# Optimization experiments

Measured on AMD Instinct MI355X. Metric: run time of the kernel, lower is better.

## Reference

```python
import jax, jax.numpy as jnp
import numpy as np
jax.config.update("jax_enable_x64", True)

B, N, FEAT_DIM, OUT_DIM = 16, 10000, 256, 256
CH = [3, 64, 64, 64, 128, FEAT_DIM]  # ptlk PointNet_features MLP widths (scale=1)
BN_EPS = 1e-5
L2_EPS = 1e-12


def setup_inputs() -> dict:
    key = jax.random.key(0)
    ks = jax.random.split(key, 2 * len(CH) + 4)
    inp = {"points": jax.random.normal(ks[0], (B, N, 3), dtype=jnp.float32)}
    for i in range(5):
        cin, cout = CH[i], CH[i + 1]
        inp[f"W{i}"] = jax.random.normal(ks[1 + 2 * i], (cout, cin), dtype=jnp.float32) / np.sqrt(cin).astype(np.float32)
        inp[f"g{i}"] = jnp.ones((cout,), jnp.float32)
        inp[f"b{i}"] = jnp.zeros((cout,), jnp.float32)
    inp["Wfc"] = jax.random.normal(ks[-2], (OUT_DIM, FEAT_DIM * FEAT_DIM), dtype=jnp.float32) / np.sqrt(FEAT_DIM * FEAT_DIM).astype(np.float32)
    inp["bfc"] = jnp.zeros((OUT_DIM,), jnp.float32)
    return inp


def _bn_relu(y, g, b):
    # training-mode BatchNorm1d over (batch, points) per channel; y: [B,C,N]
    mu = jnp.mean(y, axis=(0, 2), keepdims=True)
    var = jnp.var(y, axis=(0, 2), keepdims=True)
    y = (y - mu) * jax.lax.rsqrt(var + BN_EPS)
    return jax.nn.relu(y * g[None, :, None] + b[None, :, None])


def reference(points, W0, g0, b0, W1, g1, b1, W2, g2, b2, W3, g3, b3, W4, g4, b4, Wfc, bfc):
    x = jnp.transpose(points, (0, 2, 1))  # [B,3,N]
    for W, g, b in ((W0, g0, b0), (W1, g1, b1), (W2, g2, b2), (W3, g3, b3), (W4, g4, b4)):
        x = jnp.einsum('oc,bcn->bon', W, x)  # 1x1 conv1d
        x = _bn_relu(x, g, b)
    f = jnp.transpose(x, (0, 2, 1))  # [B,N,D] per-point features
    # so_cov: global mean over all B*N points (as in the original), then per-batch covariance
    mean = jnp.mean(f.reshape(-1, FEAT_DIM), axis=0)  # [D]
    fc = f - mean
    cov = jnp.einsum('bnd,bne->bde', fc, fc) / np.float32(N)  # [B,D,D]
    # matrix square-root via fp64 SVD (torch: x.double(); u s v = svd; u diag(s^0.5) v^T)
    u, s, vh = jnp.linalg.svd(cov.astype(jnp.float64), full_matrices=False)
    sqrt_cov = (u * jnp.sqrt(s)[:, None, :]) @ vh  # [B,D,D]
    v = sqrt_cov.reshape(f.shape[0], FEAT_DIM * FEAT_DIM).astype(jnp.float32)
    out = v @ Wfc.T + bfc  # [B,OUT_DIM]
    norm = jnp.maximum(jnp.linalg.norm(out, axis=-1, keepdims=True), L2_EPS)
    return out / norm
```

## Files before the change

kernel.cpp:

```cpp
#include <hip/hip_runtime.h>
#include <cmath>

constexpr int NB   = 16;
constexpr int NPTS = 10000;
constexpr int NBN  = NB * NPTS;
constexpr int NS_ITERS = 18;
constexpr int COV_CHUNKS = 20;
constexpr int CHUNK_PTS  = 500;
constexpr int COV_KK     = 16;

typedef _Float16 f16x8 __attribute__((ext_vector_type(8)));
typedef float  f32x4  __attribute__((ext_vector_type(4)));
typedef unsigned short ushort4v __attribute__((ext_vector_type(4)));
typedef unsigned short ushort8v __attribute__((ext_vector_type(8)));

__global__ __launch_bounds__(256) void conv0_ker(const float* __restrict__ pts,
                                                 const float* __restrict__ W,
                                                 float* __restrict__ y) {
    int g = blockIdx.x * 256 + threadIdx.x;
    int b = g / NPTS;
    int n = g - b * NPTS;
    float p0 = pts[3 * (size_t)g + 0];
    float p1 = pts[3 * (size_t)g + 1];
    float p2 = pts[3 * (size_t)g + 2];
    float* yp = y + ((size_t)b * 64) * NPTS + n;
    for (int o = 0; o < 64; ++o) {
        float v = W[3 * o] * p0 + W[3 * o + 1] * p1 + W[3 * o + 2] * p2;
        yp[(size_t)o * NPTS] = v;
    }
}

__device__ __forceinline__ unsigned short f2h(float f) {
    return __builtin_bit_cast(unsigned short, (_Float16)f);
}
__device__ __forceinline__ float hres(float f) {
    return f - (float)(_Float16)f;
}
__device__ __forceinline__ int swzu(int us) {
    return us ^ (((us >> 7) & 3) << 4);
}
__device__ __forceinline__ int swz8(int byteoff) {
    return byteoff ^ (((byteoff >> 8) & 3) << 5);
}

template <int CIN, int COUT, int OTILE>
__global__ __launch_bounds__(256) void conv_mfma(const float* __restrict__ xin,
                                                 const float* __restrict__ ss,
                                                 const float* __restrict__ W,
                                                 float* __restrict__ y,
                                                 float* __restrict__ stats) {
    constexpr int OT = OTILE / 16;
    constexpr int WM = 4;
    constexpr int WN = (OTILE == 128) ? 4 : 2;
    constexpr int NCW = (OTILE == 128) ? 2 : 4;
    __shared__ unsigned short Xp[2][8 * 512];
    __shared__ unsigned short Wp[2][OT * 512];

    const int tid  = threadIdx.x;
    const int lane = tid & 63;
    const int w    = tid >> 6;
    const int wr   = (OTILE == 128) ? (w & 1) : 0;
    const int wc   = (OTILE == 128) ? (w >> 1) : w;

    const int nb = blockIdx.x * 128;
    const int ob = blockIdx.y * OTILE;
    const int b  = blockIdx.z;

    f32x4 acc[WM][WN];
#pragma unroll
    for (int m = 0; m < WM; ++m)
#pragma unroll
        for (int n = 0; n < WN; ++n) acc[m][n] = (f32x4){0.f, 0.f, 0.f, 0.f};

    const int xn = tid & 127;
    const int th = tid >> 7;
    const bool nok = (nb + xn) < NPTS;

    float xv[2][8];
    {
        const float* xb0 = xin + ((size_t)(b * CIN)) * NPTS + nb + xn;
#pragma unroll
        for (int qq = 0; qq < 2; ++qq) {
            int q = th * 2 + qq;
#pragma unroll
            for (int j = 0; j < 8; ++j)
                xv[qq][j] = nok ? xb0[(size_t)(q * 8 + j) * NPTS] : 0.f;
        }
    }

#pragma unroll 1
    for (int kc = 0; kc < CIN; kc += 32) {
        __builtin_amdgcn_sched_barrier(0);
        __builtin_amdgcn_s_barrier();
        __builtin_amdgcn_sched_barrier(0);
#pragma unroll
        for (int i = 0; i < OTILE / 32; ++i) {
            int l = i * 256 + tid;
            int o = l >> 3, k4 = (l & 7) << 2;
            float4 v = *(const float4*)(W + (size_t)(ob + o) * CIN + kc + k4);
            ushort4v h4, l4;
            h4[0] = f2h(v.x); l4[0] = f2h(hres(v.x));
            h4[1] = f2h(v.y); l4[1] = f2h(hres(v.y));
            h4[2] = f2h(v.z); l4[2] = f2h(hres(v.z));
            h4[3] = f2h(v.w); l4[3] = f2h(hres(v.w));
            int us = swzu((o >> 4) * 512 + ((k4 >> 3) * 16 + (o & 15)) * 8 + (k4 & 7));
            *(ushort4v*)&Wp[0][us] = h4;
            *(ushort4v*)&Wp[1][us] = l4;
        }
#pragma unroll
        for (int qq = 0; qq < 2; ++qq) {
            int q = th * 2 + qq;
            float f[8];
#pragma unroll
            for (int j = 0; j < 8; ++j) {
                int c = kc + q * 8 + j;
                f[j] = fmaxf(fmaf(xv[qq][j], ss[c], ss[256 + c]), 0.f);
            }
            ushort8v h8, l8;
#pragma unroll
            for (int j = 0; j < 8; ++j) {
                h8[j] = f2h(f[j]);
                l8[j] = f2h(hres(f[j]));
            }
            int us = swzu((xn >> 4) * 512 + (q * 16 + (xn & 15)) * 8);
            *(ushort8v*)&Xp[0][us] = h8;
            *(ushort8v*)&Xp[1][us] = l8;
        }
        if (kc + 32 < CIN) {
            const float* xb0 = xin + ((size_t)(b * CIN + kc + 32)) * NPTS + nb + xn;
#pragma unroll
            for (int qq = 0; qq < 2; ++qq) {
                int q = th * 2 + qq;
#pragma unroll
                for (int j = 0; j < 8; ++j)
                    xv[qq][j] = nok ? xb0[(size_t)(q * 8 + j) * NPTS] : 0.f;
            }
        }
        asm volatile("s_waitcnt lgkmcnt(0)" ::: "memory");
        __builtin_amdgcn_s_barrier();
        __builtin_amdgcn_sched_barrier(0);

        f16x8 ah[WM], al[WM], bh[WN], bl[WN];
#pragma unroll
        for (int m = 0; m < WM; ++m) {
            int us = swzu((wr * WM + m) * 512 + lane * 8);
            ah[m] = *(const f16x8*)&Wp[0][us];
            al[m] = *(const f16x8*)&Wp[1][us];
        }
#pragma unroll
        for (int n = 0; n < WN; ++n) {
            int us = swzu((wc * WN + n) * 512 + lane * 8);
            bh[n] = *(const f16x8*)&Xp[0][us];
            bl[n] = *(const f16x8*)&Xp[1][us];
        }
#pragma unroll
        for (int m = 0; m < WM; ++m)
#pragma unroll
            for (int n = 0; n < WN; ++n) {
                acc[m][n] = __builtin_amdgcn_mfma_f32_16x16x32_f16(ah[m], bh[n], acc[m][n], 0, 0, 0);
                acc[m][n] = __builtin_amdgcn_mfma_f32_16x16x32_f16(ah[m], bl[n], acc[m][n], 0, 0, 0);
                acc[m][n] = __builtin_amdgcn_mfma_f32_16x16x32_f16(al[m], bh[n], acc[m][n], 0, 0, 0);
            }
    }

    const int ro = (lane >> 4) * 4;
    const int co = lane & 15;
#pragma unroll
    for (int m = 0; m < WM; ++m) {
        int o = ob + wr * (WM * 16) + m * 16 + ro;
#pragma unroll
        for (int n = 0; n < WN; ++n) {
            int col = nb + wc * (WN * 16) + n * 16 + co;
            if (col < NPTS) {
                float* yp = y + ((size_t)(b * COUT + o)) * NPTS + col;
#pragma unroll
                for (int r = 0; r < 4; ++r)
                    yp[(size_t)r * NPTS] = acc[m][n][r];
            }
        }
    }

    __syncthreads();
    float* sbuf = (float*)&Xp[0][0];
    float* qbuf = sbuf + NCW * OTILE;
#pragma unroll
    for (int m = 0; m < WM; ++m)
#pragma unroll
        for (int r = 0; r < 4; ++r) {
            float s = 0.f, q = 0.f;
#pragma unroll
            for (int n = 0; n < WN; ++n) {
                int col = nb + wc * (WN * 16) + n * 16 + co;
                float v = acc[m][n][r];
                if (col < NPTS) { s += v; q = fmaf(v, v, q); }
            }
            s += __shfl_xor(s, 1); q += __shfl_xor(q, 1);
            s += __shfl_xor(s, 2); q += __shfl_xor(q, 2);
            s += __shfl_xor(s, 4); q += __shfl_xor(q, 4);
            s += __shfl_xor(s, 8); q += __shfl_xor(q, 8);
            if (co == 0) {
                int rowl = wr * (WM * 16) + m * 16 + ro + r;
                sbuf[wc * OTILE + rowl] = s;
                qbuf[wc * OTILE + rowl] = q;
            }
        }
    __syncthreads();
    if (tid < OTILE) {
        float s = 0.f, q = 0.f;
#pragma unroll
        for (int j = 0; j < NCW; ++j) {
            s += sbuf[j * OTILE + tid];
            q += qbuf[j * OTILE + tid];
        }
        atomicAdd(&stats[ob + tid], s);
        atomicAdd(&stats[COUT + ob + tid], q);
    }
}

__global__ void chan_stats(const float* __restrict__ y, int C, float* __restrict__ stats) {
    int c = blockIdx.x, b = blockIdx.y, t = threadIdx.x;
    const float* p = y + ((size_t)(b * C + c)) * NPTS;
    float s = 0.f, q = 0.f;
    for (int n = t; n < NPTS; n += 256) {
        float v = p[n];
        s += v;
        q = fmaf(v, v, q);
    }
    for (int off = 32; off; off >>= 1) {
        s += __shfl_down(s, off);
        q += __shfl_down(q, off);
    }
    __shared__ float ls[4], lq[4];
    if ((t & 63) == 0) { ls[t >> 6] = s; lq[t >> 6] = q; }
    __syncthreads();
    if (t == 0) {
        atomicAdd(&stats[c],     ls[0] + ls[1] + ls[2] + ls[3]);
        atomicAdd(&stats[C + c], lq[0] + lq[1] + lq[2] + lq[3]);
    }
}

__global__ void bn_finalize(const float* __restrict__ stats, const float* __restrict__ g,
                            const float* __restrict__ bi, int C, float* __restrict__ ss) {
    int c = threadIdx.x;
    if (c < C) {
        float mu  = stats[c] * (1.f / NBN);
        float var = stats[C + c] * (1.f / NBN) - mu * mu;
        float r = rsqrtf(var + 1e-5f);
        float s = g[c] * r;
        ss[c] = s;
        ss[256 + c] = bi[c] - mu * s;
    }
}

template <int NPAN>
__device__ __forceinline__ void cov_issue(const float* __restrict__ y4, int b,
                                          int ti, int tj, int chb, int p4,
                                          int n0c, int kk, float4 (&cur)[NPAN][4]) {
    const int nbase = n0c + kk * 32;
#pragma unroll
    for (int p = 0; p < NPAN; ++p) {
        const int pcb = (p ? tj : ti) * 128;
#pragma unroll
        for (int i = 0; i < 4; ++i) {
            const int ch = chb + 32 * i;
            float4 v = make_float4(0.f, 0.f, 0.f, 0.f);
            if (kk * 32 + p4 < CHUNK_PTS)
                v = *(const float4*)(y4 + ((size_t)(b * 256 + pcb + ch)) * NPTS + nbase + p4);
            cur[p][i] = v;
        }
    }
}

template <int NPAN>
__global__ __launch_bounds__(256) void cov_mfma(const float* __restrict__ y4,
                                                const float* __restrict__ ss,
                                                float* __restrict__ covP,
                                                float* __restrict__ fsumb) {
    __shared__ unsigned short pan[NPAN][2][4096];

    const int chunk = blockIdx.x;
    const int tile  = (NPAN == 2) ? 2 : (int)blockIdx.y;
    const int b     = blockIdx.z;
    const int ti = (tile == 1) ? 1 : 0;
    const int tj = (tile == 0) ? 0 : 1;

    const int tid  = threadIdx.x;
    const int lane = tid & 63;
    const int w    = tid >> 6;
    const int wr   = w & 1, wc = w >> 1;
    const int n0c  = chunk * CHUNK_PTS;

    f32x4 acc[4][4];
#pragma unroll
    for (int m = 0; m < 4; ++m)
#pragma unroll
        for (int n = 0; n < 4; ++n) acc[m][n] = (f32x4){0.f, 0.f, 0.f, 0.f};

    const int g   = tid & 7;
    const int chb = tid >> 3;
    const int p4  = g * 4;
    const int q   = p4 >> 3, j0 = p4 & 7;

    float fs[4] = {0.f, 0.f, 0.f, 0.f};
    float4 cur[NPAN][4];

    cov_issue<NPAN>(y4, b, ti, tj, chb, p4, n0c, 0, cur);

#pragma unroll 1
    for (int kk = 0; kk < COV_KK; ++kk) {
        __builtin_amdgcn_sched_barrier(0);
        __builtin_amdgcn_s_barrier();
        __builtin_amdgcn_sched_barrier(0);

        const bool ok = (kk * 32 + p4 < CHUNK_PTS);
#pragma unroll
        for (int p = 0; p < NPAN; ++p) {
            const int pcb = (p ? tj : ti) * 128;
#pragma unroll
            for (int i = 0; i < 4; ++i) {
                const int ch = chb + 32 * i;
                float4 v = cur[p][i];
                if (ok) {
                    float sc = ss[pcb + ch], sh = ss[256 + pcb + ch];
                    v.x = fmaxf(fmaf(v.x, sc, sh), 0.f);
                    v.y = fmaxf(fmaf(v.y, sc, sh), 0.f);
                    v.z = fmaxf(fmaf(v.z, sc, sh), 0.f);
                    v.w = fmaxf(fmaf(v.w, sc, sh), 0.f);
                } else {
                    v = make_float4(0.f, 0.f, 0.f, 0.f);
                }
                if (NPAN == 1) fs[i] += (v.x + v.y) + (v.z + v.w);
                ushort4v h4, l4;
                h4[0] = f2h(v.x); l4[0] = f2h(hres(v.x));
                h4[1] = f2h(v.y); l4[1] = f2h(hres(v.y));
                h4[2] = f2h(v.z); l4[2] = f2h(hres(v.z));
                h4[3] = f2h(v.w); l4[3] = f2h(hres(v.w));
                const int addr = (ch >> 4) * 512 + (q * 16 + (ch & 15)) * 8 + j0;
                const int sa = swz8(addr * 2) >> 1;
                *(ushort4v*)&pan[p][0][sa] = h4;
                *(ushort4v*)&pan[p][1][sa] = l4;
            }
        }
        if (kk + 1 < COV_KK)
            cov_issue<NPAN>(y4, b, ti, tj, chb, p4, n0c, kk + 1, cur);

        asm volatile("s_waitcnt lgkmcnt(0)" ::: "memory");
        __builtin_amdgcn_s_barrier();
        __builtin_amdgcn_sched_barrier(0);

        const unsigned short* Ah = pan[0][0];
        const unsigned short* Al = pan[0][1];
        const unsigned short* Bh = pan[NPAN - 1][0];
        const unsigned short* Bl = pan[NPAN - 1][1];

        f16x8 ah[4], al[4], bh[4], bl[4];
#pragma unroll
        for (int m = 0; m < 4; ++m) {
            int t8 = (wr * 4 + m) * 512 + lane * 8;
            int sa = swz8(t8 * 2) >> 1;
            ah[m] = *(const f16x8*)&Ah[sa];
            al[m] = *(const f16x8*)&Al[sa];
        }
#pragma unroll
        for (int n = 0; n < 4; ++n) {
            int t8 = (wc * 4 + n) * 512 + lane * 8;
            int sa = swz8(t8 * 2) >> 1;
            bh[n] = *(const f16x8*)&Bh[sa];
            bl[n] = *(const f16x8*)&Bl[sa];
        }
#pragma unroll
        for (int m = 0; m < 4; ++m)
#pragma unroll
            for (int n = 0; n < 4; ++n) {
                acc[m][n] = __builtin_amdgcn_mfma_f32_16x16x32_f16(ah[m], bh[n], acc[m][n], 0, 0, 0);
                acc[m][n] = __builtin_amdgcn_mfma_f32_16x16x32_f16(ah[m], bl[n], acc[m][n], 0, 0, 0);
                acc[m][n] = __builtin_amdgcn_mfma_f32_16x16x32_f16(al[m], bh[n], acc[m][n], 0, 0, 0);
            }
    }

    if (NPAN == 1) {
#pragma unroll
        for (int i = 0; i < 4; ++i) {
            float s = fs[i];
            s += __shfl_xor(s, 1);
            s += __shfl_xor(s, 2);
            s += __shfl_xor(s, 4);
            if (g == 0)
                atomicAdd(&fsumb[b * 256 + ti * 128 + chb + 32 * i], s);
        }
    }

    float* outp = covP + (((size_t)(chunk * NB + b) * 3 + tile) << 14);
    const int rowb = wr * 64;
    const int colb = wc * 64;
#pragma unroll
    for (int m = 0; m < 4; ++m)
#pragma unroll
        for (int n = 0; n < 4; ++n)
#pragma unroll
            for (int r = 0; r < 4; ++r) {
                int row = rowb + m * 16 + (lane >> 4) * 4 + r;
                int col = colb + n * 16 + (lane & 15);
                outp[(row << 7) + col] = acc[m][n][r];
            }
}

__global__ void covfin_ker(const float* __restrict__ covP, const float* __restrict__ fsumb,
                           float* __restrict__ Y0, float* __restrict__ trace) {
    int r = blockIdx.x, b = blockIdx.y, c = threadIdx.x;
    float fbr = fsumb[b * 256 + r] * (1.f / NPTS);
    float fbc = fsumb[b * 256 + c] * (1.f / NPTS);
    float mr = 0.f, mc = 0.f;
    for (int q = 0; q < NB; ++q) {
        mr += fsumb[q * 256 + r];
        mc += fsumb[q * 256 + c];
    }
    mr *= (1.f / NBN);
    mc *= (1.f / NBN);
    int tile, rr, cc;
    if (r < 128 && c < 128)        { tile = 0; rr = r;       cc = c; }
    else if (r >= 128 && c >= 128) { tile = 1; rr = r - 128; cc = c - 128; }
    else if (r < 128)              { tile = 2; rr = r;       cc = c - 128; }
    else                           { tile = 2; rr = c;       cc = r - 128; }
    size_t base = (((size_t)b * 3 + tile) << 14) + ((size_t)rr << 7) + cc;
    float m5 = 0.f;
#pragma unroll
    for (int q = 0; q < COV_CHUNKS; ++q)
        m5 += covP[(size_t)q * (NB * 3 * 16384) + base];
    float v = m5 * (1.f / NPTS) - fbr * mc - mr * fbc + mr * mc;
    Y0[((size_t)b << 16) + ((size_t)r << 8) + c] = v;
    if (c == r) atomicAdd(&trace[b], v);
}

__global__ void ns_init(float* __restrict__ Y0, float* __restrict__ Z0,
                        const float* __restrict__ trace) {
    int i = blockIdx.x * 256 + threadIdx.x;
    int b = i >> 16, rc = i & 65535;
    float inv = 1.f / trace[b];
    Y0[i] *= inv;
    Z0[i] = ((rc >> 8) == (rc & 255)) ? 1.f : 0.f;
}

__device__ __forceinline__ void ns_body8(const float* __restrict__ Ab,
                                         const float* __restrict__ Bb,
                                         float* __restrict__ Ob,
                                         float scale, float diag, int tile, int tid,
                                         unsigned short* Ap0, unsigned short* Ap1,
                                         unsigned short* Bp0, unsigned short* Bp1) {
    const int lane = tid & 63;
    const int w    = tid >> 6;
    const int wr   = w & 3;
    const int wc   = w >> 2;
    const int tr = (tile >> 2) * 64, tc = (tile & 3) * 64;

    f32x4 acc[2];
    acc[0] = (f32x4){0.f, 0.f, 0.f, 0.f};
    acc[1] = (f32x4){0.f, 0.f, 0.f, 0.f};

    const int r2   = tid >> 3;
    const int kq8  = tid & 7;
    const int colB = tid & 63;
    const int kB   = tid >> 6;

#pragma unroll 1
    for (int kc = 0; kc < 256; kc += 64) {
        __syncthreads();
        {
            const float* ap = Ab + (size_t)(tr + r2) * 256 + kc + kq8 * 8;
            float av[8];
            *(float4*)&av[0] = *(const float4*)ap;
            *(float4*)&av[4] = *(const float4*)(ap + 4);
            ushort8v h8, l8;
#pragma unroll
            for (int j = 0; j < 8; ++j) { h8[j] = f2h(av[j]); l8[j] = f2h(hres(av[j])); }
            const int ua = ((r2 >> 4) * 2 + (kq8 >> 2)) * 512 + ((kq8 & 3) * 16 + (r2 & 15)) * 8;
            const int sa = swz8(ua * 2) >> 1;
            *(ushort8v*)&Ap0[sa] = h8;
            *(ushort8v*)&Ap1[sa] = l8;
        }
        {
            const float* bp = Bb + (size_t)(kc + kB * 8) * 256 + tc + colB;
            float bv[8];
#pragma unroll
            for (int j = 0; j < 8; ++j) bv[j] = bp[(size_t)j * 256];
            ushort8v h8, l8;
#pragma unroll
            for (int j = 0; j < 8; ++j) { h8[j] = f2h(bv[j]); l8[j] = f2h(hres(bv[j])); }
            const int ub = ((colB >> 4) * 2 + (kB >> 2)) * 512 + ((kB & 3) * 16 + (colB & 15)) * 8;
            const int sb = swz8(ub * 2) >> 1;
            *(ushort8v*)&Bp0[sb] = h8;
            *(ushort8v*)&Bp1[sb] = l8;
        }
        __syncthreads();

#pragma unroll
        for (int kk = 0; kk < 2; ++kk) {
            const int ua = swz8(((wr * 2 + kk) * 512 + lane * 8) * 2) >> 1;
            f16x8 a_h = *(const f16x8*)&Ap0[ua];
            f16x8 a_l = *(const f16x8*)&Ap1[ua];
#pragma unroll
            for (int n = 0; n < 2; ++n) {
                const int ub = swz8((((wc * 2 + n) * 2 + kk) * 512 + lane * 8) * 2) >> 1;
                f16x8 b_h = *(const f16x8*)&Bp0[ub];
                f16x8 b_l = *(const f16x8*)&Bp1[ub];
                acc[n] = __builtin_amdgcn_mfma_f32_16x16x32_f16(a_h, b_h, acc[n], 0, 0, 0);
                acc[n] = __builtin_amdgcn_mfma_f32_16x16x32_f16(a_h, b_l, acc[n], 0, 0, 0);
                acc[n] = __builtin_amdgcn_mfma_f32_16x16x32_f16(a_l, b_h, acc[n], 0, 0, 0);
            }
        }
    }

    const int ro = (lane >> 4) * 4, co = lane & 15;
#pragma unroll
    for (int n = 0; n < 2; ++n) {
        int row = tr + wr * 16 + ro;
        int col = tc + wc * 32 + n * 16 + co;
#pragma unroll
        for (int r = 0; r < 4; ++r) {
            float v = scale * acc[n][r] + (((row + r) == col) ? diag : 0.f);
            Ob[(size_t)(row + r) * 256 + col] = v;
        }
    }
}

__global__ __launch_bounds__(512) void ns_gemm(const float* __restrict__ A,
                                               const float* __restrict__ B,
                                               float* __restrict__ O,
                                               float scale, float diag) {
    __shared__ unsigned short Ap[2][4096], Bp[2][4096];
    size_t off = (size_t)blockIdx.y << 16;
    ns_body8(A + off, B + off, O + off, scale, diag, blockIdx.x, threadIdx.x,
             Ap[0], Ap[1], Bp[0], Bp[1]);
}

__global__ __launch_bounds__(512) void ns_gemm_pair(const float* __restrict__ Y,
                                                    const float* __restrict__ Mm,
                                                    const float* __restrict__ Z,
                                                    float* __restrict__ Yn,
                                                    float* __restrict__ Zn) {
    __shared__ unsigned short Ap[2][4096], Bp[2][4096];
    size_t off = (size_t)blockIdx.y << 16;
    if (blockIdx.z == 0)
        ns_body8(Y + off, Mm + off, Yn + off, 0.5f, 0.f, blockIdx.x, threadIdx.x,
                 Ap[0], Ap[1], Bp[0], Bp[1]);
    else
        ns_body8(Mm + off, Z + off, Zn + off, 0.5f, 0.f, blockIdx.x, threadIdx.x,
                 Ap[0], Ap[1], Bp[0], Bp[1]);
}

__global__ __launch_bounds__(256) void fc_ker(const float* __restrict__ Yf,
                                              const float* __restrict__ trace,
                                              const float* __restrict__ Wfc,
                                              float* __restrict__ outpre) {
    int kc = blockIdx.x;
    int ot = blockIdx.y;
    int t = threadIdx.x;
    __shared__ float Wl[64][129];
    __shared__ float Vl[16][129];
#pragma unroll
    for (int i = 0; i < 32; ++i) {
        int l = i * 256 + t;
        int o = l >> 7, k = l & 127;
        Wl[o][k] = Wfc[(size_t)(ot * 64 + o) * 65536 + kc * 128 + k];
    }
#pragma unroll
    for (int i = 0; i < 8; ++i) {
        int l = i * 256 + t;
        int bb = l >> 7, k = l & 127;
        Vl[bb][k] = sqrtf(trace[bb]) * Yf[((size_t)bb << 16) + kc * 128 + k];
    }
    __syncthreads();
    int ol = t & 63, bg = t >> 6;
    float a0 = 0.f, a1 = 0.f, a2 = 0.f, a3 = 0.f;
    for (int k = 0; k < 128; ++k) {
        float w = Wl[ol][k];
        a0 = fmaf(w, Vl[bg * 4 + 0][k], a0);
        a1 = fmaf(w, Vl[bg * 4 + 1][k], a1);
        a2 = fmaf(w, Vl[bg * 4 + 2][k], a2);
        a3 = fmaf(w, Vl[bg * 4 + 3][k], a3);
    }
    int o = ot * 64 + ol;
    atomicAdd(&outpre[(bg * 4 + 0) * 256 + o], a0);
    atomicAdd(&outpre[(bg * 4 + 1) * 256 + o], a1);
    atomicAdd(&outpre[(bg * 4 + 2) * 256 + o], a2);
    atomicAdd(&outpre[(bg * 4 + 3) * 256 + o], a3);
}

__global__ void norm_ker(const float* __restrict__ outpre, const float* __restrict__ bfc,
                         float* __restrict__ dout) {
    int b = blockIdx.x, t = threadIdx.x;
    float v = outpre[b * 256 + t] + bfc[t];
    float q = v * v;
    for (int off = 32; off; off >>= 1) q += __shfl_xor(q, off);
    __shared__ float lq[4];
    __shared__ float snorm;
    if ((t & 63) == 0) lq[t >> 6] = q;
    __syncthreads();
    if (t == 0) snorm = fmaxf(sqrtf(lq[0] + lq[1] + lq[2] + lq[3]), 1e-12f);
    __syncthreads();
    dout[b * 256 + t] = v / snorm;
}

extern "C" void kernel_launch(void* const* d_in, const int* in_sizes, int n_in,
                              void* d_out, int out_size, void* d_ws, size_t ws_size,
                              hipStream_t stream) {
    (void)in_sizes; (void)n_in; (void)out_size; (void)ws_size;
    const float* pts = (const float*)d_in[0];
    const float* Wm[5]; const float* gm[5]; const float* bm[5];
    for (int i = 0; i < 5; ++i) {
        Wm[i] = (const float*)d_in[1 + 3 * i];
        gm[i] = (const float*)d_in[2 + 3 * i];
        bm[i] = (const float*)d_in[3 + 3 * i];
    }
    const float* Wfc = (const float*)d_in[16];
    const float* bfc = (const float*)d_in[17];

    float* ws     = (float*)d_ws;
    float* stats  = ws;
    float* fsumb  = ws + 2560;
    float* trace  = ws + 6656;
    float* outpre = ws + 6672;
    float* ss     = ws + 10768;
    float* R      = ws + 16384;
    float* P      = R;
    float* Q      = R + (size_t)NB * 256 * NPTS;
    float* covP   = Q;
    float* Y0     = R;
    float* Y1     = Y0 + 1048576;
    float* Z0     = Y1 + 1048576;
    float* Z1     = Z0 + 1048576;
    float* Mb     = Z1 + 1048576;

    hipMemsetAsync(ws, 0, 16384 * sizeof(float), stream);

    conv0_ker<<<dim3(NBN / 256), dim3(256), 0, stream>>>(pts, Wm[0], P);
    chan_stats<<<dim3(64, NB), dim3(256), 0, stream>>>(P, 64, stats);
    bn_finalize<<<dim3(1), dim3(256), 0, stream>>>(stats, gm[0], bm[0], 64, ss);
    conv_mfma<64, 64, 64><<<dim3(79, 1, NB), dim3(256), 0, stream>>>(P, ss, Wm[1], Q, stats + 512);
    bn_finalize<<<dim3(1), dim3(256), 0, stream>>>(stats + 512, gm[1], bm[1], 64, ss + 512);
    conv_mfma<64, 64, 64><<<dim3(79, 1, NB), dim3(256), 0, stream>>>(Q, ss + 512, Wm[2], P, stats + 1024);
    bn_finalize<<<dim3(1), dim3(256), 0, stream>>>(stats + 1024, gm[2], bm[2], 64, ss + 1024);
    conv_mfma<64, 128, 128><<<dim3(79, 1, NB), dim3(256), 0, stream>>>(P, ss + 1024, Wm[3], Q, stats + 1536);
    bn_finalize<<<dim3(1), dim3(256), 0, stream>>>(stats + 1536, gm[3], bm[3], 128, ss + 1536);
    conv_mfma<128, 256, 128><<<dim3(79, 2, NB), dim3(256), 0, stream>>>(Q, ss + 1536, Wm[4], R, stats + 2048);
    bn_finalize<<<dim3(1), dim3(256), 0, stream>>>(stats + 2048, gm[4], bm[4], 256, ss + 2048);

    cov_mfma<1><<<dim3(COV_CHUNKS, 2, NB), dim3(256), 0, stream>>>(R, ss + 2048, covP, fsumb);
    cov_mfma<2><<<dim3(COV_CHUNKS, 1, NB), dim3(256), 0, stream>>>(R, ss + 2048, covP, fsumb);
    covfin_ker<<<dim3(256, NB), dim3(256), 0, stream>>>(covP, fsumb, Y0, trace);
    ns_init<<<dim3(4096), dim3(256), 0, stream>>>(Y0, Z0, trace);

    float* Yc = Y0; float* Zc = Z0; float* Yn = Y1; float* Zn = Z1;
    for (int it = 0; it < NS_ITERS; ++it) {
        ns_gemm<<<dim3(16, NB), dim3(512), 0, stream>>>(Zc, Yc, Mb, -1.f, 3.f);
        ns_gemm_pair<<<dim3(16, NB, 2), dim3(512), 0, stream>>>(Yc, Mb, Zc, Yn, Zn);
        float* ty = Yc; Yc = Yn; Yn = ty;
        float* tz = Zc; Zc = Zn; Zn = tz;
    }

    fc_ker<<<dim3(512, 4), dim3(256), 0, stream>>>(Yc, trace, Wfc, outpre);
    norm_ker<<<dim3(NB), dim3(256), 0, stream>>>(outpre, bfc, (float*)d_out);
}
```

Baseline: 949.3 us.

## Remap NS GEMM blocks to XCDs per batch and drop conv register prefetch

The Newton-Schulz GEMM kernels now use a 1D grid whose block index is decoded so that all tiles of a given batch matrix land on the same XCD under round-robin dispatch. The aim is better L2 reuse of each 256x256 matrix across its 16 tiles. Separately, the conv MFMA kernel drops its register-level prefetch of the next K-chunk of activations and replaces the hand-placed barriers with __syncthreads. That second change lowers register pressure but puts global load latency back on the critical path.

```diff
diff --git a/kernel.cpp b/kernel.cpp
--- a/kernel.cpp
+++ b/kernel.cpp
@@ -76,23 +76,9 @@
     const int th = tid >> 7;
     const bool nok = (nb + xn) < NPTS;
 
-    float xv[2][8];
-    {
-        const float* xb0 = xin + ((size_t)(b * CIN)) * NPTS + nb + xn;
-#pragma unroll
-        for (int qq = 0; qq < 2; ++qq) {
-            int q = th * 2 + qq;
-#pragma unroll
-            for (int j = 0; j < 8; ++j)
-                xv[qq][j] = nok ? xb0[(size_t)(q * 8 + j) * NPTS] : 0.f;
-        }
-    }
-
 #pragma unroll 1
     for (int kc = 0; kc < CIN; kc += 32) {
-        __builtin_amdgcn_sched_barrier(0);
-        __builtin_amdgcn_s_barrier();
-        __builtin_amdgcn_sched_barrier(0);
+        __syncthreads();
 #pragma unroll
         for (int i = 0; i < OTILE / 32; ++i) {
             int l = i * 256 + tid;
@@ -110,11 +96,13 @@
 #pragma unroll
         for (int qq = 0; qq < 2; ++qq) {
             int q = th * 2 + qq;
+            const float* xb = xin + ((size_t)(b * CIN + kc + q * 8)) * NPTS + nb + xn;
             float f[8];
 #pragma unroll
             for (int j = 0; j < 8; ++j) {
+                float v = nok ? xb[(size_t)j * NPTS] : 0.f;
                 int c = kc + q * 8 + j;
-                f[j] = fmaxf(fmaf(xv[qq][j], ss[c], ss[256 + c]), 0.f);
+                f[j] = fmaxf(fmaf(v, ss[c], ss[256 + c]), 0.f);
             }
             ushort8v h8, l8;
 #pragma unroll
@@ -126,19 +114,7 @@
             *(ushort8v*)&Xp[0][us] = h8;
             *(ushort8v*)&Xp[1][us] = l8;
         }
-        if (kc + 32 < CIN) {
-            const float* xb0 = xin + ((size_t)(b * CIN + kc + 32)) * NPTS + nb + xn;
-#pragma unroll
-            for (int qq = 0; qq < 2; ++qq) {
-                int q = th * 2 + qq;
-#pragma unroll
-                for (int j = 0; j < 8; ++j)
-                    xv[qq][j] = nok ? xb0[(size_t)(q * 8 + j) * NPTS] : 0.f;
-            }
-        }
-        asm volatile("s_waitcnt lgkmcnt(0)" ::: "memory");
-        __builtin_amdgcn_s_barrier();
-        __builtin_amdgcn_sched_barrier(0);
+        __syncthreads();
 
         f16x8 ah[WM], al[WM], bh[WN], bl[WN];
 #pragma unroll
@@ -528,8 +504,13 @@
                                                float* __restrict__ O,
                                                float scale, float diag) {
     __shared__ unsigned short Ap[2][4096], Bp[2][4096];
-    size_t off = (size_t)blockIdx.y << 16;
-    ns_body8(A + off, B + off, O + off, scale, diag, blockIdx.x, threadIdx.x,
+    const int id  = blockIdx.x;
+    const int xcd = id & 7;
+    const int k   = id >> 3;
+    const int b   = 2 * xcd + (k >> 4);
+    const int tile = k & 15;
+    size_t off = (size_t)b << 16;
+    ns_body8(A + off, B + off, O + off, scale, diag, tile, threadIdx.x,
              Ap[0], Ap[1], Bp[0], Bp[1]);
 }
 
@@ -539,12 +520,19 @@
                                                     float* __restrict__ Yn,
                                                     float* __restrict__ Zn) {
     __shared__ unsigned short Ap[2][4096], Bp[2][4096];
-    size_t off = (size_t)blockIdx.y << 16;
-    if (blockIdx.z == 0)
-        ns_body8(Y + off, Mm + off, Yn + off, 0.5f, 0.f, blockIdx.x, threadIdx.x,
+    const int id  = blockIdx.x;
+    const int xcd = id & 7;
+    const int k   = id >> 3;
+    const int z   = k >> 5;
+    const int rem = k & 31;
+    const int b   = 2 * xcd + (rem >> 4);
+    const int tile = rem & 15;
+    size_t off = (size_t)b << 16;
+    if (z == 0)
+        ns_body8(Y + off, Mm + off, Yn + off, 0.5f, 0.f, tile, threadIdx.x,
                  Ap[0], Ap[1], Bp[0], Bp[1]);
     else
-        ns_body8(Mm + off, Z + off, Zn + off, 0.5f, 0.f, blockIdx.x, threadIdx.x,
+        ns_body8(Mm + off, Z + off, Zn + off, 0.5f, 0.f, tile, threadIdx.x,
                  Ap[0], Ap[1], Bp[0], Bp[1]);
 }
 
@@ -652,8 +640,8 @@
 
     float* Yc = Y0; float* Zc = Z0; float* Yn = Y1; float* Zn = Z1;
     for (int it = 0; it < NS_ITERS; ++it) {
-        ns_gemm<<<dim3(16, NB), dim3(512), 0, stream>>>(Zc, Yc, Mb, -1.f, 3.f);
-        ns_gemm_pair<<<dim3(16, NB, 2), dim3(512), 0, stream>>>(Yc, Mb, Zc, Yn, Zn);
+        ns_gemm<<<dim3(256), dim3(512), 0, stream>>>(Zc, Yc, Mb, -1.f, 3.f);
+        ns_gemm_pair<<<dim3(512), dim3(512), 0, stream>>>(Yc, Mb, Zc, Yn, Zn);
         float* ty = Yc; Yc = Yn; Yn = ty;
         float* tz = Zc; Zc = Zn; Zn = tz;
     }
```

New measurement: 844.9 us. 1.12x faster.
